# Kernel optimization log

Measured on AMD Instinct MI355X. Metric: run time of the kernel, lower is better.

Reference implementation:

```python
import jax, jax.numpy as jnp
import numpy as np

B, S, D = 4, 2048, 768
LN_EPS = 1e-12


def setup_inputs() -> dict:
    key = jax.random.key(0)
    k0, k1, k2, k3 = jax.random.split(key, 4)
    scale = 1.0 / np.sqrt(D).astype(np.float32)
    return {
        "hidden_states": jax.random.normal(k0, (B, S, D), jnp.float32),
        "attention_mask": jnp.ones((B, 1, S, S), jnp.int32),
        "prior_n_attn": jax.random.uniform(k1, (B, S, S), jnp.float32),
        "ln_w": jnp.ones((D,), jnp.float32),
        "ln_b": jnp.zeros((D,), jnp.float32),
        "wq": jax.random.normal(k2, (D, D), jnp.float32) * scale,
        "bq": jnp.zeros((D,), jnp.float32),
        "wk": jax.random.normal(k3, (D, D), jnp.float32) * scale,
        "bk": jnp.zeros((D,), jnp.float32),
    }


def reference(hidden_states, attention_mask, prior_n_attn, ln_w, ln_b, wq, bq, wk, bk):
    _, S_, D_ = hidden_states.shape
    # LayerNorm (biased variance, as torch.nn.LayerNorm)
    mu = hidden_states.mean(-1, keepdims=True)
    var = ((hidden_states - mu) ** 2).mean(-1, keepdims=True)
    h = (hidden_states - mu) / jnp.sqrt(var + LN_EPS) * ln_w + ln_b

    a = jnp.eye(S_, k=1, dtype=jnp.int32)      # superdiagonal
    bI = jnp.eye(S_, dtype=jnp.int32)          # diagonal
    c = jnp.eye(S_, k=-1, dtype=jnp.int32)     # subdiagonal
    tri = jnp.triu(jnp.ones((S_, S_), jnp.float32))

    # mask & (a + c): band of width 1 off the diagonal; then squeeze dim 1
    mask = (attention_mask.astype(jnp.int32) & (a + c))[:, 0]  # [B,S,S]

    q = h @ wq + bq
    k = h @ wk + bk
    scores = jnp.einsum("bsd,btd->bst", q, k) / D_
    scores = jnp.where(mask == 0, -jnp.inf, scores)
    n = jnp.nan_to_num(jax.nn.softmax(scores, axis=-1))
    n = jnp.sqrt(n * jnp.swapaxes(n, -2, -1) + 1e-9)
    n = prior_n_attn + (1.0 - prior_n_attn) * n

    # keep only the superdiagonal of log(n + 1e-9); zero elsewhere
    logm = jnp.log(n + 1e-9) * a.astype(n.dtype)
    # prefix-sum via triangular matmuls (same math as torch source)
    t = logm @ tri                                   # [B,S,S]
    g = jnp.exp(jnp.einsum("ij,bjk->bik", tri, t))   # [B,S,S]
    su = tri - bI.astype(tri.dtype)                  # strictly-upper indicator
    g = g * su                                       # masked_fill((tri-b)==0, 0)
    diag_part = jnp.where(bI == 0, 1e-9, n)          # n.masked_fill(b==0, 1e-9)
    g = g + jnp.swapaxes(g, -2, -1) + diag_part
    return (g, n)
```

## Files before the change

### kernel.cpp

```cpp
#include <hip/hip_runtime.h>
#include <hip/hip_bf16.h>
#include <math.h>
#include <stdint.h>

#define BB 4
#define SS 2048
#define DD 768
#define NN 1536
#define MM (BB*SS)

typedef __attribute__((ext_vector_type(4))) float  f32x4;
typedef __attribute__((ext_vector_type(8))) __bf16 bf16x8;
typedef __attribute__((ext_vector_type(4))) __bf16 bf16x4;

#define AS1 __attribute__((address_space(1)))
#define AS3 __attribute__((address_space(3)))

__global__ __launch_bounds__(192) void ln_kernel(const float* __restrict__ x,
        const float* __restrict__ lw, const float* __restrict__ lb,
        __bf16* __restrict__ h) {
    const int row = blockIdx.x;
    const int t = threadIdx.x;
    const float* xr = x + (size_t)row * DD;
    f32x4 v = *(const f32x4*)(xr + t * 4);
    float s  = v[0] + v[1] + v[2] + v[3];
    float ss = v[0]*v[0] + v[1]*v[1] + v[2]*v[2] + v[3]*v[3];
#pragma unroll
    for (int o = 1; o < 64; o <<= 1) { s += __shfl_xor(s, o); ss += __shfl_xor(ss, o); }
    __shared__ float smS[3], smQ[3];
    if ((t & 63) == 0) { smS[t >> 6] = s; smQ[t >> 6] = ss; }
    __syncthreads();
    float tS = smS[0] + smS[1] + smS[2];
    float tQ = smQ[0] + smQ[1] + smQ[2];
    float mu  = tS * (1.0f / DD);
    float var = tQ * (1.0f / DD) - mu * mu;
    float rstd = 1.0f / sqrtf(var + 1e-12f);
    f32x4 wv = *(const f32x4*)(lw + t * 4);
    f32x4 bv = *(const f32x4*)(lb + t * 4);
    bf16x4 o;
#pragma unroll
    for (int c = 0; c < 4; c++) {
        float y = (v[c] - mu) * rstd * wv[c] + bv[c];
        o[c] = (__bf16)y;
    }
    *(bf16x4*)(h + (size_t)row * DD + t * 4) = o;
}

__global__ __launch_bounds__(256) void wt_kernel(const float* __restrict__ wq,
        const float* __restrict__ wk, __bf16* __restrict__ Wt) {
    __shared__ float tile[64][65];
    const int n0 = blockIdx.x * 64;
    const int k0 = blockIdx.y * 64;
    const float* src = (n0 < DD) ? wq : wk;
    const int nc = (n0 < DD) ? n0 : (n0 - DD);
    for (int e = threadIdx.x; e < 64 * 64; e += 256) {
        int r = e >> 6, c = e & 63;
        tile[r][c] = src[(size_t)(k0 + r) * DD + nc + c];
    }
    __syncthreads();
    for (int e = threadIdx.x; e < 64 * 64; e += 256) {
        int r = e >> 6, c = e & 63;
        Wt[(size_t)(n0 + r) * DD + k0 + c] = (__bf16)tile[c][r];
    }
}

__global__ __launch_bounds__(256) void gemm_kernel(const __bf16* __restrict__ A,
        const __bf16* __restrict__ Bt,
        const float* __restrict__ bq, const float* __restrict__ bk,
        float* __restrict__ C) {
    __shared__ __attribute__((aligned(16))) __bf16 As[128][32];
    __shared__ __attribute__((aligned(16))) __bf16 Bs[128][32];
    const int m0 = blockIdx.x * 128;
    const int n0 = blockIdx.y * 128;
    const int t = threadIdx.x;
    const int wave = t >> 6, lane = t & 63;
    const int wr = wave >> 1, wc = wave & 1;
    f32x4 acc[4][4] = {};

    char* asb = (char*)&As[0][0];
    char* bsb = (char*)&Bs[0][0];
    const int c0  = wave * 64 + lane;
    const int rA0 = c0 >> 2;
    const int cA0 = (c0 & 3) << 3;

    for (int k0 = 0; k0 < DD; k0 += 32) {
        const __bf16* ga0 = A  + (size_t)(m0 + rA0) * DD + k0 + cA0;
        const __bf16* ga1 = ga0 + (size_t)64 * DD;
        const __bf16* gb0 = Bt + (size_t)(n0 + rA0) * DD + k0 + cA0;
        const __bf16* gb1 = gb0 + (size_t)64 * DD;
        __builtin_amdgcn_global_load_lds((const AS1 void*)(ga0), (AS3 void*)(asb + wave * 1024),        16, 0, 0);
        __builtin_amdgcn_global_load_lds((const AS1 void*)(ga1), (AS3 void*)(asb + 4096 + wave * 1024), 16, 0, 0);
        __builtin_amdgcn_global_load_lds((const AS1 void*)(gb0), (AS3 void*)(bsb + wave * 1024),        16, 0, 0);
        __builtin_amdgcn_global_load_lds((const AS1 void*)(gb1), (AS3 void*)(bsb + 4096 + wave * 1024), 16, 0, 0);
        __syncthreads();
        const int r = lane & 15, ko = (lane >> 4) << 3;
        bf16x8 af[4], bvf[4];
#pragma unroll
        for (int i = 0; i < 4; i++) af[i]  = *(const bf16x8*)&As[wr * 64 + i * 16 + r][ko];
#pragma unroll
        for (int j = 0; j < 4; j++) bvf[j] = *(const bf16x8*)&Bs[wc * 64 + j * 16 + r][ko];
#pragma unroll
        for (int i = 0; i < 4; i++)
#pragma unroll
            for (int j = 0; j < 4; j++)
                acc[i][j] = __builtin_amdgcn_mfma_f32_16x16x32_bf16(af[i], bvf[j], acc[i][j], 0, 0, 0);
        __syncthreads();
    }
#pragma unroll
    for (int i = 0; i < 4; i++) {
        const int mm = m0 + wr * 64 + i * 16 + (lane >> 4) * 4;
#pragma unroll
        for (int j = 0; j < 4; j++) {
            const int nn = n0 + wc * 64 + j * 16 + (lane & 15);
            const float bias = (nn < DD) ? bq[nn] : bk[nn - DD];
#pragma unroll
            for (int rr = 0; rr < 4; rr++)
                C[(size_t)(mm + rr) * NN + nn] = acc[i][j][rr] + bias;
        }
    }
}

__global__ __launch_bounds__(256) void band_kernel(const float* __restrict__ QK,
        const int* __restrict__ att, float* __restrict__ pu, float* __restrict__ pd) {
    const int idx  = blockIdx.x * 4 + (threadIdx.x >> 6);
    const int lane = threadIdx.x & 63;
    const int b = idx >> 11;
    const int s = idx & 2047;
    const float* q = QK + (size_t)idx * NN;
    float qv[12];
#pragma unroll
    for (int m = 0; m < 12; m++) qv[m] = q[lane + 64 * m];
    float du = 0.f, dn = 0.f;
    if (s < SS - 1) {
        const float* kk = QK + (size_t)(idx + 1) * NN + DD;
#pragma unroll
        for (int m = 0; m < 12; m++) du += qv[m] * kk[lane + 64 * m];
    }
    if (s > 0) {
        const float* kk = QK + (size_t)(idx - 1) * NN + DD;
#pragma unroll
        for (int m = 0; m < 12; m++) dn += qv[m] * kk[lane + 64 * m];
    }
#pragma unroll
    for (int o = 1; o < 64; o <<= 1) { du += __shfl_xor(du, o); dn += __shfl_xor(dn, o); }
    if (lane == 0) {
        const float eu = du * (1.0f / DD), ed = dn * (1.0f / DD);
        const bool au = (s < SS - 1) && ((att[((size_t)b * SS + s) * SS + (s + 1)] & 1) != 0);
        const bool ad = (s > 0)      && ((att[((size_t)b * SS + s) * SS + (s - 1)] & 1) != 0);
        float puv = 0.f, pdv = 0.f;
        if (au || ad) {
            float mx = au ? eu : ed;
            if (au && ad) mx = fmaxf(eu, ed);
            const float zu = au ? expf(eu - mx) : 0.f;
            const float zd = ad ? expf(ed - mx) : 0.f;
            const float iz = 1.f / (zu + zd);
            puv = zu * iz; pdv = zd * iz;
        }
        pu[idx] = puv; pd[idx] = pdv;
    }
}

__global__ __launch_bounds__(256) void scan_kernel(const float* __restrict__ pu,
        const float* __restrict__ pd, const float* __restrict__ prior,
        float* __restrict__ nb, double* __restrict__ P) {
    const int b = blockIdx.x;
    const int t = threadIdx.x;
    double L[8];
    double mysum = 0.0;
#pragma unroll
    for (int e = 0; e < 8; e++) {
        const int s = t * 8 + e;
        double Lv = 0.0;
        float nbv = 0.f;
        if (s < SS - 1) {
            const float a = pu[b * SS + s];
            const float c = pd[b * SS + s + 1];
            nbv = sqrtf(a * c + 1e-9f);
            const float pr = prior[(size_t)b * SS * SS + (size_t)s * SS + s + 1];
            const float nsup = pr + (1.f - pr) * nbv;
            Lv = log((double)nsup + 1e-9);
        }
        nb[b * SS + s] = nbv;
        L[e] = Lv; mysum += Lv;
    }
    __shared__ double warr[256];
    warr[t] = mysum;
    __syncthreads();
    for (int o = 1; o < 256; o <<= 1) {
        double v = 0.0;
        if (t >= o) v = warr[t - o];
        __syncthreads();
        if (t >= o) warr[t] += v;
        __syncthreads();
    }
    double run = warr[t] - mysum;
#pragma unroll
    for (int e = 0; e < 8; e++) {
        P[(size_t)b * SS + t * 8 + e] = run;
        run += L[e];
    }
}

__global__ __launch_bounds__(256) void out_kernel(const float* __restrict__ prior,
        const float* __restrict__ nb, const double* __restrict__ P,
        float* __restrict__ gout, float* __restrict__ nout) {
    const size_t f = (size_t)blockIdx.x * 256 + threadIdx.x;
    const int b = (int)(f >> 20);
    const size_t r = f & 1048575;
    const int i  = (int)(r >> 9);
    const int k4 = (int)(r & 511) * 4;
    const f32x4 pv = *(const f32x4*)(prior + (f << 2));
    const double Pi = P[(size_t)b * SS + i];
    f32x4 nres, gres;
#pragma unroll
    for (int c = 0; c < 4; c++) {
        const int k = k4 + c;
        const float pr = pv[c];
        float v = 3.16227766016838e-5f;
        if (k == i + 1)      v = nb[b * SS + i];
        else if (k == i - 1) v = nb[b * SS + k];
        const float nval = pr + (1.f - pr) * v;
        nres[c] = nval;
        float g;
        if (k == i) {
            g = nval;
        } else {
            const double Pk = P[(size_t)b * SS + k];
            const double dd = (k > i) ? (Pk - Pi) : (Pi - Pk);
            g = expf((float)dd) + 1e-9f;
        }
        gres[c] = g;
    }
    *(f32x4*)(gout + (f << 2)) = gres;
    *(f32x4*)(nout + (f << 2)) = nres;
}

extern "C" void kernel_launch(void* const* d_in, const int* in_sizes, int n_in,
                              void* d_out, int out_size, void* d_ws, size_t ws_size,
                              hipStream_t stream) {
    const float* hs    = (const float*)d_in[0];
    const int*   att   = (const int*)d_in[1];
    const float* prior = (const float*)d_in[2];
    const float* ln_w  = (const float*)d_in[3];
    const float* ln_b  = (const float*)d_in[4];
    const float* wq    = (const float*)d_in[5];
    const float* bq    = (const float*)d_in[6];
    const float* wk    = (const float*)d_in[7];
    const float* bk    = (const float*)d_in[8];

    float* gout = (float*)d_out;
    float* nout = gout + (size_t)BB * SS * SS;

    char* ws = (char*)d_ws;
    __bf16* h   = (__bf16*)(ws);
    __bf16* Wt  = (__bf16*)(ws + 12582912);
    float*  QK  = (float*)(ws + 14942208);
    float*  pu  = (float*)(ws + 65273856);
    float*  pd  = (float*)(ws + 65306624);
    float*  nb  = (float*)(ws + 65339392);
    double* P   = (double*)(ws + 65372160);

    ln_kernel<<<dim3(MM), dim3(192), 0, stream>>>(hs, ln_w, ln_b, h);
    wt_kernel<<<dim3(NN / 64, DD / 64), dim3(256), 0, stream>>>(wq, wk, Wt);
    gemm_kernel<<<dim3(MM / 128, NN / 128), dim3(256), 0, stream>>>(h, Wt, bq, bk, QK);
    band_kernel<<<dim3(MM / 4), dim3(256), 0, stream>>>(QK, att, pu, pd);
    scan_kernel<<<dim3(BB), dim3(256), 0, stream>>>(pu, pd, prior, nb, P);
    out_kernel<<<dim3((BB * SS * SS / 4) / 256), dim3(256), 0, stream>>>(prior, nb, P, gout, nout);
}
```

Before: 114.6 us.

## Fold Wq·Wkᵀ into one matrix so band scores need a single GEMM

Rewrites the band scores q_s·k_t as h_s·(Wq Wkᵀ)·h_t plus bias terms. It precomputes G = Wq·Wkᵀ (768x768), forms R = h·G in bf16, and takes rank-1 bias corrections from the LayerNorm kernel. This halves the big GEMM's N dimension from 1536 to 768 and replaces the fp32 QK intermediate with a bf16 R, cutting GEMM FLOPs and band-kernel memory traffic. The cost is an extra small GEMM, extra kernel launches, and more bf16 rounding (G and R are stored in bf16), which adds numerical error.

Result: faster. 110.8 us (-3.3%).

```diff
diff --git a/kernel.cpp b/kernel.cpp
--- a/kernel.cpp
+++ b/kernel.cpp
@@ -6,7 +6,6 @@
 #define BB 4
 #define SS 2048
 #define DD 768
-#define NN 1536
 #define MM (BB*SS)
 
 typedef __attribute__((ext_vector_type(4))) float  f32x4;
@@ -16,58 +15,99 @@
 #define AS1 __attribute__((address_space(1)))
 #define AS3 __attribute__((address_space(3)))
 
-__global__ __launch_bounds__(192) void ln_kernel(const float* __restrict__ x,
+__global__ __launch_bounds__(256) void wcvt_kernel(const float* __restrict__ wq,
+        const float* __restrict__ wk, __bf16* __restrict__ Wqb, __bf16* __restrict__ Wkb) {
+    const int bid = blockIdx.x;
+    const float* src; __bf16* dst; int off;
+    if (bid < 576) { src = wq; dst = Wqb; off = bid; }
+    else           { src = wk; dst = Wkb; off = bid - 576; }
+    const size_t e = ((size_t)off * 256 + threadIdx.x) * 4;
+    f32x4 v = *(const f32x4*)(src + e);
+    bf16x4 o;
+#pragma unroll
+    for (int c = 0; c < 4; c++) o[c] = (__bf16)v[c];
+    *(bf16x4*)(dst + e) = o;
+}
+
+__global__ __launch_bounds__(256) void uvcb_kernel(const float* __restrict__ wq,
+        const float* __restrict__ wk, const float* __restrict__ bq,
+        const float* __restrict__ bk, float* __restrict__ u, float* __restrict__ v,
+        float* __restrict__ cb) {
+    const int bid = blockIdx.x;
+    const int lane = threadIdx.x & 63, wv = threadIdx.x >> 6;
+    if (bid == 384) {
+        if (wv != 0) return;
+        float s = 0.f;
+#pragma unroll
+        for (int m = 0; m < 12; m++) s += bq[lane + 64 * m] * bk[lane + 64 * m];
+#pragma unroll
+        for (int o = 1; o < 64; o <<= 1) s += __shfl_xor(s, o);
+        if (lane == 0) cb[0] = s;
+        return;
+    }
+    const bool isU = bid < 192;
+    const int row = (isU ? bid : bid - 192) * 4 + wv;
+    const float* W = isU ? wq : wk;
+    const float* bvec = isU ? bk : bq;
+    const float* wr = W + (size_t)row * DD;
+    float s = 0.f;
+#pragma unroll
+    for (int m = 0; m < 12; m++) s += wr[lane + 64 * m] * bvec[lane + 64 * m];
+#pragma unroll
+    for (int o = 1; o < 64; o <<= 1) s += __shfl_xor(s, o);
+    if (lane == 0) (isU ? u : v)[row] = s;
+}
+
+__global__ __launch_bounds__(256) void ln_kernel(const float* __restrict__ x,
         const float* __restrict__ lw, const float* __restrict__ lb,
-        __bf16* __restrict__ h) {
-    const int row = blockIdx.x;
-    const int t = threadIdx.x;
-    const float* xr = x + (size_t)row * DD;
-    f32x4 v = *(const f32x4*)(xr + t * 4);
-    float s  = v[0] + v[1] + v[2] + v[3];
-    float ss = v[0]*v[0] + v[1]*v[1] + v[2]*v[2] + v[3]*v[3];
+        const float* __restrict__ u, const float* __restrict__ v,
+        __bf16* __restrict__ h, float* __restrict__ Aarr, float* __restrict__ Barr) {
+    const int row = blockIdx.x * 4 + (threadIdx.x >> 6);
+    const int lane = threadIdx.x & 63;
+    const float* xr = x + (size_t)row * DD + lane * 12;
+    f32x4 a0 = *(const f32x4*)(xr), a1 = *(const f32x4*)(xr + 4), a2 = *(const f32x4*)(xr + 8);
+    float xs[12];
+#pragma unroll
+    for (int c = 0; c < 4; c++) { xs[c] = a0[c]; xs[4 + c] = a1[c]; xs[8 + c] = a2[c]; }
+    float s = 0.f, ss = 0.f;
+#pragma unroll
+    for (int c = 0; c < 12; c++) { s += xs[c]; ss += xs[c] * xs[c]; }
 #pragma unroll
     for (int o = 1; o < 64; o <<= 1) { s += __shfl_xor(s, o); ss += __shfl_xor(ss, o); }
-    __shared__ float smS[3], smQ[3];
-    if ((t & 63) == 0) { smS[t >> 6] = s; smQ[t >> 6] = ss; }
-    __syncthreads();
-    float tS = smS[0] + smS[1] + smS[2];
-    float tQ = smQ[0] + smQ[1] + smQ[2];
-    float mu  = tS * (1.0f / DD);
-    float var = tQ * (1.0f / DD) - mu * mu;
-    float rstd = 1.0f / sqrtf(var + 1e-12f);
-    f32x4 wv = *(const f32x4*)(lw + t * 4);
-    f32x4 bv = *(const f32x4*)(lb + t * 4);
-    bf16x4 o;
+    const float mu = s * (1.0f / DD);
+    const float var = ss * (1.0f / DD) - mu * mu;
+    const float rstd = 1.0f / sqrtf(var + 1e-12f);
+    const float* wp = lw + lane * 12; const float* bp = lb + lane * 12;
+    const float* up = u + lane * 12;  const float* vp = v + lane * 12;
+    f32x4 w0 = *(const f32x4*)(wp), w1 = *(const f32x4*)(wp + 4), w2 = *(const f32x4*)(wp + 8);
+    f32x4 b0 = *(const f32x4*)(bp), b1 = *(const f32x4*)(bp + 4), b2 = *(const f32x4*)(bp + 8);
+    f32x4 u0 = *(const f32x4*)(up), u1 = *(const f32x4*)(up + 4), u2 = *(const f32x4*)(up + 8);
+    f32x4 v0 = *(const f32x4*)(vp), v1 = *(const f32x4*)(vp + 4), v2 = *(const f32x4*)(vp + 8);
+    float wv[12], bv[12], uv[12], vv[12];
 #pragma unroll
     for (int c = 0; c < 4; c++) {
-        float y = (v[c] - mu) * rstd * wv[c] + bv[c];
-        o[c] = (__bf16)y;
-    }
-    *(bf16x4*)(h + (size_t)row * DD + t * 4) = o;
-}
-
-__global__ __launch_bounds__(256) void wt_kernel(const float* __restrict__ wq,
-        const float* __restrict__ wk, __bf16* __restrict__ Wt) {
-    __shared__ float tile[64][65];
-    const int n0 = blockIdx.x * 64;
-    const int k0 = blockIdx.y * 64;
-    const float* src = (n0 < DD) ? wq : wk;
-    const int nc = (n0 < DD) ? n0 : (n0 - DD);
-    for (int e = threadIdx.x; e < 64 * 64; e += 256) {
-        int r = e >> 6, c = e & 63;
-        tile[r][c] = src[(size_t)(k0 + r) * DD + nc + c];
-    }
-    __syncthreads();
-    for (int e = threadIdx.x; e < 64 * 64; e += 256) {
-        int r = e >> 6, c = e & 63;
-        Wt[(size_t)(n0 + r) * DD + k0 + c] = (__bf16)tile[c][r];
-    }
-}
-
-__global__ __launch_bounds__(256) void gemm_kernel(const __bf16* __restrict__ A,
-        const __bf16* __restrict__ Bt,
-        const float* __restrict__ bq, const float* __restrict__ bk,
-        float* __restrict__ C) {
+        wv[c] = w0[c]; wv[4 + c] = w1[c]; wv[8 + c] = w2[c];
+        bv[c] = b0[c]; bv[4 + c] = b1[c]; bv[8 + c] = b2[c];
+        uv[c] = u0[c]; uv[4 + c] = u1[c]; uv[8 + c] = u2[c];
+        vv[c] = v0[c]; vv[4 + c] = v1[c]; vv[8 + c] = v2[c];
+    }
+    bf16x4 o0, o1, o2;
+    float ap = 0.f, bpv = 0.f;
+#pragma unroll
+    for (int c = 0; c < 12; c++) {
+        const float y = (xs[c] - mu) * rstd * wv[c] + bv[c];
+        ap += y * uv[c]; bpv += y * vv[c];
+        if (c < 4) o0[c] = (__bf16)y; else if (c < 8) o1[c - 4] = (__bf16)y; else o2[c - 8] = (__bf16)y;
+    }
+    __bf16* hr = h + (size_t)row * DD + lane * 12;
+    *(bf16x4*)(hr) = o0; *(bf16x4*)(hr + 4) = o1; *(bf16x4*)(hr + 8) = o2;
+#pragma unroll
+    for (int o = 1; o < 64; o <<= 1) { ap += __shfl_xor(ap, o); bpv += __shfl_xor(bpv, o); }
+    if (lane == 0) { Aarr[row] = ap; Barr[row] = bpv; }
+}
+
+__global__ __launch_bounds__(256) void gemm768_kernel(const __bf16* __restrict__ A,
+        const __bf16* __restrict__ Bt, __bf16* __restrict__ C) {
     __shared__ __attribute__((aligned(16))) __bf16 As[128][32];
     __shared__ __attribute__((aligned(16))) __bf16 Bs[128][32];
     const int m0 = blockIdx.x * 128;
@@ -112,39 +152,54 @@
 #pragma unroll
         for (int j = 0; j < 4; j++) {
             const int nn = n0 + wc * 64 + j * 16 + (lane & 15);
-            const float bias = (nn < DD) ? bq[nn] : bk[nn - DD];
 #pragma unroll
             for (int rr = 0; rr < 4; rr++)
-                C[(size_t)(mm + rr) * NN + nn] = acc[i][j][rr] + bias;
-        }
-    }
-}
-
-__global__ __launch_bounds__(256) void band_kernel(const float* __restrict__ QK,
-        const int* __restrict__ att, float* __restrict__ pu, float* __restrict__ pd) {
+                C[(size_t)(mm + rr) * DD + nn] = (__bf16)acc[i][j][rr];
+        }
+    }
+}
+
+__global__ __launch_bounds__(256) void band_kernel(const __bf16* __restrict__ h,
+        const __bf16* __restrict__ R, const int* __restrict__ att,
+        const float* __restrict__ Aarr, const float* __restrict__ Barr,
+        const float* __restrict__ cbp, float* __restrict__ pu, float* __restrict__ pd) {
     const int idx  = blockIdx.x * 4 + (threadIdx.x >> 6);
     const int lane = threadIdx.x & 63;
     const int b = idx >> 11;
     const int s = idx & 2047;
-    const float* q = QK + (size_t)idx * NN;
-    float qv[12];
-#pragma unroll
-    for (int m = 0; m < 12; m++) qv[m] = q[lane + 64 * m];
+    const __bf16* hp = h + (size_t)idx * DD + lane * 12;
+    bf16x4 h0 = *(const bf16x4*)(hp), h1 = *(const bf16x4*)(hp + 4), h2 = *(const bf16x4*)(hp + 8);
+    float hv[12];
+#pragma unroll
+    for (int c = 0; c < 4; c++) { hv[c] = (float)h0[c]; hv[4 + c] = (float)h1[c]; hv[8 + c] = (float)h2[c]; }
     float du = 0.f, dn = 0.f;
     if (s < SS - 1) {
-        const float* kk = QK + (size_t)(idx + 1) * NN + DD;
-#pragma unroll
-        for (int m = 0; m < 12; m++) du += qv[m] * kk[lane + 64 * m];
+        const __bf16* rp = R + (size_t)(idx + 1) * DD + lane * 12;
+        bf16x4 r0 = *(const bf16x4*)(rp), r1 = *(const bf16x4*)(rp + 4), r2 = *(const bf16x4*)(rp + 8);
+#pragma unroll
+        for (int c = 0; c < 4; c++) {
+            du += hv[c] * (float)r0[c];
+            du += hv[4 + c] * (float)r1[c];
+            du += hv[8 + c] * (float)r2[c];
+        }
     }
     if (s > 0) {
-        const float* kk = QK + (size_t)(idx - 1) * NN + DD;
-#pragma unroll
-        for (int m = 0; m < 12; m++) dn += qv[m] * kk[lane + 64 * m];
+        const __bf16* rp = R + (size_t)(idx - 1) * DD + lane * 12;
+        bf16x4 r0 = *(const bf16x4*)(rp), r1 = *(const bf16x4*)(rp + 4), r2 = *(const bf16x4*)(rp + 8);
+#pragma unroll
+        for (int c = 0; c < 4; c++) {
+            dn += hv[c] * (float)r0[c];
+            dn += hv[4 + c] * (float)r1[c];
+            dn += hv[8 + c] * (float)r2[c];
+        }
     }
 #pragma unroll
     for (int o = 1; o < 64; o <<= 1) { du += __shfl_xor(du, o); dn += __shfl_xor(dn, o); }
     if (lane == 0) {
-        const float eu = du * (1.0f / DD), ed = dn * (1.0f / DD);
+        const float cb = cbp[0];
+        const float As = Aarr[idx];
+        const float eu = (du + As + ((s < SS - 1) ? Barr[idx + 1] : 0.f) + cb) * (1.0f / DD);
+        const float ed = (dn + As + ((s > 0)      ? Barr[idx - 1] : 0.f) + cb) * (1.0f / DD);
         const bool au = (s < SS - 1) && ((att[((size_t)b * SS + s) * SS + (s + 1)] & 1) != 0);
         const bool ad = (s > 0)      && ((att[((size_t)b * SS + s) * SS + (s - 1)] & 1) != 0);
         float puv = 0.f, pdv = 0.f;
@@ -252,18 +307,27 @@
     float* nout = gout + (size_t)BB * SS * SS;
 
     char* ws = (char*)d_ws;
-    __bf16* h   = (__bf16*)(ws);
-    __bf16* Wt  = (__bf16*)(ws + 12582912);
-    float*  QK  = (float*)(ws + 14942208);
-    float*  pu  = (float*)(ws + 65273856);
-    float*  pd  = (float*)(ws + 65306624);
-    float*  nb  = (float*)(ws + 65339392);
-    double* P   = (double*)(ws + 65372160);
-
-    ln_kernel<<<dim3(MM), dim3(192), 0, stream>>>(hs, ln_w, ln_b, h);
-    wt_kernel<<<dim3(NN / 64, DD / 64), dim3(256), 0, stream>>>(wq, wk, Wt);
-    gemm_kernel<<<dim3(MM / 128, NN / 128), dim3(256), 0, stream>>>(h, Wt, bq, bk, QK);
-    band_kernel<<<dim3(MM / 4), dim3(256), 0, stream>>>(QK, att, pu, pd);
-    scan_kernel<<<dim3(BB), dim3(256), 0, stream>>>(pu, pd, prior, nb, P);
-    out_kernel<<<dim3((BB * SS * SS / 4) / 256), dim3(256), 0, stream>>>(prior, nb, P, gout, nout);
-}
+    __bf16* h    = (__bf16*)(ws);
+    __bf16* Wqb  = (__bf16*)(ws + 12582912);
+    __bf16* Wkb  = (__bf16*)(ws + 13762560);
+    __bf16* G    = (__bf16*)(ws + 14942208);
+    __bf16* R    = (__bf16*)(ws + 16121856);
+    float*  u    = (float*) (ws + 28704768);
+    float*  v    = (float*) (ws + 28707840);
+    float*  Aarr = (float*) (ws + 28710912);
+    float*  Barr = (float*) (ws + 28743680);
+    float*  cb   = (float*) (ws + 28776448);
+    float*  pu   = (float*) (ws + 28776704);
+    float*  pd   = (float*) (ws + 28809472);
+    float*  nbuf = (float*) (ws + 28842240);
+    double* P    = (double*)(ws + 28875008);
+
+    wcvt_kernel<<<dim3(1152), dim3(256), 0, stream>>>(wq, wk, Wqb, Wkb);
+    uvcb_kernel<<<dim3(385), dim3(256), 0, stream>>>(wq, wk, bq, bk, u, v, cb);
+    ln_kernel<<<dim3(MM / 4), dim3(256), 0, stream>>>(hs, ln_w, ln_b, u, v, h, Aarr, Barr);
+    gemm768_kernel<<<dim3(6, 6), dim3(256), 0, stream>>>(Wqb, Wkb, G);
+    gemm768_kernel<<<dim3(MM / 128, 6), dim3(256), 0, stream>>>(h, G, R);
+    band_kernel<<<dim3(MM / 4), dim3(256), 0, stream>>>(h, R, att, Aarr, Barr, cb, pu, pd);
+    scan_kernel<<<dim3(BB), dim3(256), 0, stream>>>(pu, pd, prior, nbuf, P);
+    out_kernel<<<dim3((BB * SS * SS / 4) / 256), dim3(256), 0, stream>>>(prior, nbuf, P, gout, nout);
+}
```
